# Kernel optimization log

Measured on AMD Instinct MI355X. Metric: run time of the kernel, lower is better.

The kernel has to match this reference:

```python
import jax, jax.numpy as jnp
import numpy as np

MAX_DIST = 3          # census patch radius -> 7x7 neighborhood
PATCH = 2 * MAX_DIST + 1


def _warp(img, flow):
    """Bilinear warp (Resample2d): sample img at (x + u, y + v). Coords clamped to border."""
    B, C, H, W = img.shape
    gy, gx = jnp.meshgrid(jnp.arange(H, dtype=img.dtype), jnp.arange(W, dtype=img.dtype), indexing='ij')
    x = gx[None] + flow[:, 0]           # [B,H,W]
    y = gy[None] + flow[:, 1]
    x0 = jnp.floor(x); y0 = jnp.floor(y)
    wx = x - x0; wy = y - y0            # bilinear weights
    x0i = jnp.clip(x0, 0, W - 1).astype(jnp.int32)
    x1i = jnp.clip(x0 + 1.0, 0, W - 1).astype(jnp.int32)
    y0i = jnp.clip(y0, 0, H - 1).astype(jnp.int32)
    y1i = jnp.clip(y0 + 1.0, 0, H - 1).astype(jnp.int32)

    def gather(im_b, yi, xi):           # im_b [C,H,W], yi/xi [H,W] -> [C,H,W]
        return im_b[:, yi, xi]
    g = jax.vmap(gather)
    Ia = g(img, y0i, x0i); Ib = g(img, y0i, x1i)
    Ic = g(img, y1i, x0i); Id = g(img, y1i, x1i)
    wx = wx[:, None]; wy = wy[:, None]  # [B,1,H,W]
    return Ia * (1 - wx) * (1 - wy) + Ib * wx * (1 - wy) + Ic * (1 - wx) * wy + Id * wx * wy


def _census_transform(image):
    """Ternary census transform: grayscale, extract 7x7 patches, normalized center differences."""
    gray = (0.299 * image[:, 0:1] + 0.587 * image[:, 1:2] + 0.114 * image[:, 2:3]) * 255.0
    w = jnp.eye(PATCH * PATCH, dtype=image.dtype).reshape(PATCH * PATCH, 1, PATCH, PATCH)
    patches = jax.lax.conv_general_dilated(
        gray, w, window_strides=(1, 1), padding=[(MAX_DIST, MAX_DIST)] * 2,
        dimension_numbers=('NCHW', 'OIHW', 'NCHW'))   # [B,49,H,W]
    t = patches - gray
    return t / jnp.sqrt(0.81 + t * t)


def _border_mask(B, H, W, dtype):
    m = jnp.zeros((H, W), dtype).at[MAX_DIST:H - MAX_DIST, MAX_DIST:W - MAX_DIST].set(1.0)
    return jnp.broadcast_to(m[None, None], (B, 1, H, W))


def _charbonnier(x, mask, alpha=0.45, eps=0.001):
    err = (x * x + eps * eps) ** alpha * mask
    return jnp.sum(err) / x.size


def _census_loss(im1, im2_warped, mask):
    t1 = _census_transform(im1)
    t2 = _census_transform(im2_warped)
    d = (t1 - t2) ** 2
    dist = jnp.sum(d / (0.1 + d), axis=1, keepdims=True)   # soft Hamming distance [B,1,H,W]
    B, _, H, W = dist.shape
    return _charbonnier(dist, mask * _border_mask(B, H, W, dist.dtype))


def setup_inputs() -> dict:
    key = jax.random.key(0)
    ks = jax.random.split(key, 6)
    B, H, W = 4, 320, 768
    return {
        'former': jax.random.uniform(ks[0], (B, 3, H, W), jnp.float32),
        'latter': jax.random.uniform(ks[1], (B, 3, H, W), jnp.float32),
        'disp_est_scale': jax.random.normal(ks[2], (B, 2, H, W), jnp.float32) * 3.0,
        'disp_est_scale_2': jax.random.normal(ks[3], (B, 2, H, W), jnp.float32) * 3.0,
        'fw_mask': jax.random.uniform(ks[4], (B, 1, H, W), jnp.float32),
        'bw_mask': jax.random.uniform(ks[5], (B, 1, H, W), jnp.float32),
    }


def reference(former, latter, disp_est_scale, disp_est_scale_2, fw_mask, bw_mask):
    left_est = _warp(latter, disp_est_scale)
    image_loss = _census_loss(former, left_est, fw_mask)
    right_est = _warp(former, disp_est_scale_2)
    image_loss_2 = _census_loss(latter, right_est, bw_mask)
    return (image_loss, image_loss_2)
```

## Files before the change

### kernel.cpp

```cpp
#include <hip/hip_runtime.h>

#define BB 4
#define H 320
#define W 768
#define P (H*W)
#define NPIX (BB*P)
#define P4 (P/4)
#define NP4 (NPIX/4)

#define TX 32
#define TY 8
#define TW (TX+6)
#define TH (TY+6)
#define HALO (TW*TH)
#define NBX (W/TX)
#define NBY (H/TY)
#define NBLK (NBX*NBY*BB)

typedef float f4 __attribute__((ext_vector_type(4)));

__global__ __launch_bounds__(256)
void gray_kernel(const float* __restrict__ former,
                 const float* __restrict__ latter,
                 float* __restrict__ gf, float* __restrict__ gl,
                 unsigned* __restrict__ counter) {
    int idx = blockIdx.x * blockDim.x + threadIdx.x;
    if (idx == 0) *counter = 0u;
    if (idx >= NP4) return;
    int b = idx / P4;
    int r4 = idx - b * P4;
    const float* fb = former + (size_t)b * 3 * P;
    const float* lb = latter + (size_t)b * 3 * P;
    const f4 fr = *((const f4*)fb + r4);
    const f4 fg = *((const f4*)(fb + P) + r4);
    const f4 fbl = *((const f4*)(fb + 2 * P) + r4);
    const f4 lr = *((const f4*)lb + r4);
    const f4 lg = *((const f4*)(lb + P) + r4);
    const f4 lbl = *((const f4*)(lb + 2 * P) + r4);
    f4 go, lo;
#pragma unroll
    for (int k = 0; k < 4; ++k) {
        go[k] = (0.299f * fr[k] + 0.587f * fg[k] + 0.114f * fbl[k]) * 255.f;
        lo[k] = (0.299f * lr[k] + 0.587f * lg[k] + 0.114f * lbl[k]) * 255.f;
    }
    *((f4*)gf + (size_t)b * P4 + r4) = go;
    *((f4*)gl + (size_t)b * P4 + r4) = lo;
}

__device__ __forceinline__ float bilinear(const float* __restrict__ img, float fx, float fy) {
    float x0 = floorf(fx), y0 = floorf(fy);
    float wx = fx - x0, wy = fy - y0;
    float x0c = fminf(fmaxf(x0,       0.f), (float)(W - 1));
    float x1c = fminf(fmaxf(x0 + 1.f, 0.f), (float)(W - 1));
    float y0c = fminf(fmaxf(y0,       0.f), (float)(H - 1));
    float y1c = fminf(fmaxf(y0 + 1.f, 0.f), (float)(H - 1));
    int x0i = (int)x0c, x1i = (int)x1c, y0i = (int)y0c, y1i = (int)y1c;
    float Ia = img[y0i * W + x0i], Ib = img[y0i * W + x1i];
    float Ic = img[y1i * W + x0i], Id = img[y1i * W + x1i];
    float omx = 1.f - wx, omy = 1.f - wy;
    return Ia * omx * omy + Ib * wx * omy + Ic * omx * wy + Id * wx * wy;
}

__global__ __launch_bounds__(256, 5)
void fused_kernel(const float* __restrict__ gf, const float* __restrict__ gl,
                  const float* __restrict__ flow1, const float* __restrict__ flow2,
                  const float* __restrict__ fw_mask, const float* __restrict__ bw_mask,
                  float* __restrict__ partials, unsigned* __restrict__ counter,
                  float* __restrict__ out) {
    __shared__ f4 sT[HALO];
    const int b   = blockIdx.z;
    const int tx0 = blockIdx.x * TX;
    const int ty0 = blockIdx.y * TY;
    const int tid = threadIdx.x;

    const float* pGF = gf + (size_t)b * P;
    const float* pGL = gl + (size_t)b * P;
    const float* pU1 = flow1 + (size_t)b * 2 * P;
    const float* pU2 = flow2 + (size_t)b * 2 * P;

    for (int i = tid; i < HALO; i += 256) {
        int ly = i / TW, lx = i - ly * TW;
        int gx = min(max(tx0 - 3 + lx, 0), W - 1);
        int gy = min(max(ty0 - 3 + ly, 0), H - 1);
        int o = gy * W + gx;
        float A = pGF[o];
        float C = pGL[o];
        float u1 = pU1[o], v1 = pU1[P + o];
        float u2 = pU2[o], v2 = pU2[P + o];
        float Bv = bilinear(pGL, (float)gx + u1, (float)gy + v1);
        float D  = bilinear(pGF, (float)gx + u2, (float)gy + v2);
        sT[i] = (f4){A, Bv, C, D};
    }
    __syncthreads();

    const int lx = tid & 31, ly = tid >> 5;
    const int x = tx0 + lx, y = ty0 + ly;
    float sum1 = 0.f, sum2 = 0.f;

    if (x >= 3 && x < W - 3 && y >= 3 && y < H - 3) {
        const float m1 = fw_mask[(size_t)b * P + y * W + x];
        const float m2 = bw_mask[(size_t)b * P + y * W + x];
        const int c = (ly + 3) * TW + (lx + 3);
        const f4 cv = sT[c];
        const float c1 = cv.x, c2 = cv.y, c3 = cv.z, c4 = cv.w;
        float acc1a = 0.f, acc1b = 0.f, acc2a = 0.f, acc2b = 0.f;
#pragma unroll
        for (int dy = 0; dy < 7; ++dy) {
            const int ro = (ly + dy) * TW + lx;
#pragma unroll
            for (int dx = 0; dx < 7; ++dx) {
                if (dy == 3 && dx == 3) continue;
                const f4 n = sT[ro + dx];
                const float a1 = n.x - c1, b1 = n.y - c2;
                const float qa1 = fmaf(a1, a1, 0.81f), qb1 = fmaf(b1, b1, 0.81f);
                const float pr1 = qa1 * qb1;
                const float s1 = __builtin_amdgcn_rsqf(pr1);
                const float num1 = fmaf(-0.81f, qa1 + qb1, pr1 + pr1);
                const float d1 = fmaf(num1, s1 * s1, ((a1 * b1) * s1) * -2.f);
                const float a2 = n.z - c3, b2 = n.w - c4;
                const float qa2 = fmaf(a2, a2, 0.81f), qb2 = fmaf(b2, b2, 0.81f);
                const float pr2 = qa2 * qb2;
                const float s2 = __builtin_amdgcn_rsqf(pr2);
                const float num2 = fmaf(-0.81f, qa2 + qb2, pr2 + pr2);
                const float d2 = fmaf(num2, s2 * s2, ((a2 * b2) * s2) * -2.f);
                const float e1 = d1 + 0.1f, e2 = d2 + 0.1f;
                const float ir = __builtin_amdgcn_rcpf(e1 * e2);
                const float g1 = (d1 * e2) * ir;
                const float g2 = (d2 * e1) * ir;
                if (dx & 1) { acc1a += g1; acc2a += g2; }
                else        { acc1b += g1; acc2b += g2; }
            }
        }
        const float dist1 = acc1a + acc1b;
        const float dist2 = acc2a + acc2b;
        sum1 = exp2f(0.45f * log2f(fmaf(dist1, dist1, 1e-6f))) * m1;
        sum2 = exp2f(0.45f * log2f(fmaf(dist2, dist2, 1e-6f))) * m2;
    }

#pragma unroll
    for (int off = 32; off; off >>= 1) {
        sum1 += __shfl_down(sum1, off, 64);
        sum2 += __shfl_down(sum2, off, 64);
    }
    __shared__ float red[8];
    const int wave = tid >> 6, lane = tid & 63;
    if (lane == 0) { red[wave] = sum1; red[4 + wave] = sum2; }
    __syncthreads();

    __shared__ unsigned sLast;
    if (tid == 0) {
        const int blk = (blockIdx.z * NBY + blockIdx.y) * NBX + blockIdx.x;
        __hip_atomic_store(&partials[2 * blk],     red[0] + red[1] + red[2] + red[3],
                           __ATOMIC_RELAXED, __HIP_MEMORY_SCOPE_AGENT);
        __hip_atomic_store(&partials[2 * blk + 1], red[4] + red[5] + red[6] + red[7],
                           __ATOMIC_RELAXED, __HIP_MEMORY_SCOPE_AGENT);
        asm volatile("s_waitcnt vmcnt(0)" ::: "memory");
        unsigned prev = __hip_atomic_fetch_add(counter, 1u, __ATOMIC_RELAXED,
                                               __HIP_MEMORY_SCOPE_AGENT);
        sLast = (prev == NBLK - 1) ? 1u : 0u;
    }
    __syncthreads();
    if (sLast) {
        float s1 = 0.f, s2 = 0.f;
        for (int i = tid; i < NBLK; i += 256) {
            s1 += __hip_atomic_load(&partials[2 * i],     __ATOMIC_RELAXED, __HIP_MEMORY_SCOPE_AGENT);
            s2 += __hip_atomic_load(&partials[2 * i + 1], __ATOMIC_RELAXED, __HIP_MEMORY_SCOPE_AGENT);
        }
#pragma unroll
        for (int off = 32; off; off >>= 1) {
            s1 += __shfl_down(s1, off, 64);
            s2 += __shfl_down(s2, off, 64);
        }
        __shared__ float red2[8];
        if (lane == 0) { red2[wave] = s1; red2[4 + wave] = s2; }
        __syncthreads();
        if (tid == 0) {
            out[0] = (red2[0] + red2[1] + red2[2] + red2[3]) * (1.0f / NPIX);
            out[1] = (red2[4] + red2[5] + red2[6] + red2[7]) * (1.0f / NPIX);
        }
    }
}

extern "C" void kernel_launch(void* const* d_in, const int* in_sizes, int n_in,
                              void* d_out, int out_size, void* d_ws, size_t ws_size,
                              hipStream_t stream) {
    (void)in_sizes; (void)n_in; (void)out_size; (void)ws_size;
    const float* former  = (const float*)d_in[0];
    const float* latter  = (const float*)d_in[1];
    const float* flow1   = (const float*)d_in[2];
    const float* flow2   = (const float*)d_in[3];
    const float* fw_mask = (const float*)d_in[4];
    const float* bw_mask = (const float*)d_in[5];
    float* out = (float*)d_out;
    float* ws  = (float*)d_ws;
    float* gf       = ws;
    float* gl       = ws + NPIX;
    float* partials = ws + 2 * (size_t)NPIX;
    unsigned* counter = (unsigned*)(ws + 2 * (size_t)NPIX + 2 * NBLK);

    gray_kernel<<<(NP4 + 255) / 256, 256, 0, stream>>>(former, latter, gf, gl, counter);
    fused_kernel<<<dim3(NBX, NBY, BB), 256, 0, stream>>>(gf, gl, flow1, flow2,
                                                         fw_mask, bw_mask,
                                                         partials, counter, out);
}
```

Measured before the change: 144.1 us.

## Merge gray and census kernels into persistent kernel with grid barrier

Replaces the two launches with a single persistent kernel of 1280 blocks. Each block first computes a slice of the grayscale images, then all blocks meet at a global atomic barrier, and each block then loops over several census tiles. The per-neighbor soft-Hamming maths is also simplified to compute the normalized census values directly, using one rsq per operand instead of the combined product formulation. This aims to remove a kernel launch and its gap, at the cost of a spin barrier that assumes every block is co-resident, and a memset launch to reset the counters.

Result: slower. 220.4 us (+53.0%).

```diff
diff --git a/kernel.cpp b/kernel.cpp
--- a/kernel.cpp
+++ b/kernel.cpp
@@ -17,35 +17,11 @@
 #define NBY (H/TY)
 #define NBLK (NBX*NBY*BB)
 
+#define GRID 1280
+#define TPB (NBLK/GRID)
+
 typedef float f4 __attribute__((ext_vector_type(4)));
-
-__global__ __launch_bounds__(256)
-void gray_kernel(const float* __restrict__ former,
-                 const float* __restrict__ latter,
-                 float* __restrict__ gf, float* __restrict__ gl,
-                 unsigned* __restrict__ counter) {
-    int idx = blockIdx.x * blockDim.x + threadIdx.x;
-    if (idx == 0) *counter = 0u;
-    if (idx >= NP4) return;
-    int b = idx / P4;
-    int r4 = idx - b * P4;
-    const float* fb = former + (size_t)b * 3 * P;
-    const float* lb = latter + (size_t)b * 3 * P;
-    const f4 fr = *((const f4*)fb + r4);
-    const f4 fg = *((const f4*)(fb + P) + r4);
-    const f4 fbl = *((const f4*)(fb + 2 * P) + r4);
-    const f4 lr = *((const f4*)lb + r4);
-    const f4 lg = *((const f4*)(lb + P) + r4);
-    const f4 lbl = *((const f4*)(lb + 2 * P) + r4);
-    f4 go, lo;
-#pragma unroll
-    for (int k = 0; k < 4; ++k) {
-        go[k] = (0.299f * fr[k] + 0.587f * fg[k] + 0.114f * fbl[k]) * 255.f;
-        lo[k] = (0.299f * lr[k] + 0.587f * lg[k] + 0.114f * lbl[k]) * 255.f;
-    }
-    *((f4*)gf + (size_t)b * P4 + r4) = go;
-    *((f4*)gl + (size_t)b * P4 + r4) = lo;
-}
+typedef unsigned long long u64;
 
 __device__ __forceinline__ float bilinear(const float* __restrict__ img, float fx, float fy) {
     float x0 = floorf(fx), y0 = floorf(fy);
@@ -62,102 +38,149 @@
 }
 
 __global__ __launch_bounds__(256, 5)
-void fused_kernel(const float* __restrict__ gf, const float* __restrict__ gl,
-                  const float* __restrict__ flow1, const float* __restrict__ flow2,
-                  const float* __restrict__ fw_mask, const float* __restrict__ bw_mask,
-                  float* __restrict__ partials, unsigned* __restrict__ counter,
-                  float* __restrict__ out) {
+void fused_all(const float* __restrict__ former, const float* __restrict__ latter,
+               const float* __restrict__ flow1, const float* __restrict__ flow2,
+               const float* __restrict__ fw_mask, const float* __restrict__ bw_mask,
+               float* __restrict__ gf, float* __restrict__ gl,
+               float* __restrict__ partials, unsigned* __restrict__ bar,
+               unsigned* __restrict__ done, float* __restrict__ out) {
     __shared__ f4 sT[HALO];
-    const int b   = blockIdx.z;
-    const int tx0 = blockIdx.x * TX;
-    const int ty0 = blockIdx.y * TY;
+    __shared__ float red[8];
+    __shared__ unsigned sLast;
     const int tid = threadIdx.x;
-
-    const float* pGF = gf + (size_t)b * P;
-    const float* pGL = gl + (size_t)b * P;
-    const float* pU1 = flow1 + (size_t)b * 2 * P;
-    const float* pU2 = flow2 + (size_t)b * 2 * P;
-
-    for (int i = tid; i < HALO; i += 256) {
-        int ly = i / TW, lx = i - ly * TW;
-        int gx = min(max(tx0 - 3 + lx, 0), W - 1);
-        int gy = min(max(ty0 - 3 + ly, 0), H - 1);
-        int o = gy * W + gx;
-        float A = pGF[o];
-        float C = pGL[o];
-        float u1 = pU1[o], v1 = pU1[P + o];
-        float u2 = pU2[o], v2 = pU2[P + o];
-        float Bv = bilinear(pGL, (float)gx + u1, (float)gy + v1);
-        float D  = bilinear(pGF, (float)gx + u2, (float)gy + v2);
-        sT[i] = (f4){A, Bv, C, D};
-    }
+    const int wave = tid >> 6, lane = tid & 63;
+
+    {
+        int idx = blockIdx.x * 256 + tid;
+        if (idx < NP4) {
+            int b = idx / P4;
+            int r4 = idx - b * P4;
+            const float* fb = former + (size_t)b * 3 * P;
+            const float* lb = latter + (size_t)b * 3 * P;
+            const f4 fr = *((const f4*)fb + r4);
+            const f4 fg = *((const f4*)(fb + P) + r4);
+            const f4 fbl = *((const f4*)(fb + 2 * P) + r4);
+            const f4 lr = *((const f4*)lb + r4);
+            const f4 lg = *((const f4*)(lb + P) + r4);
+            const f4 lbl = *((const f4*)(lb + 2 * P) + r4);
+            union { f4 v; u64 u[2]; } cg, cl;
+#pragma unroll
+            for (int k = 0; k < 4; ++k) {
+                cg.v[k] = (0.299f * fr[k] + 0.587f * fg[k] + 0.114f * fbl[k]) * 255.f;
+                cl.v[k] = (0.299f * lr[k] + 0.587f * lg[k] + 0.114f * lbl[k]) * 255.f;
+            }
+            u64* pg = (u64*)((f4*)gf + (size_t)b * P4 + r4);
+            u64* pl = (u64*)((f4*)gl + (size_t)b * P4 + r4);
+            __hip_atomic_store(pg,     cg.u[0], __ATOMIC_RELAXED, __HIP_MEMORY_SCOPE_AGENT);
+            __hip_atomic_store(pg + 1, cg.u[1], __ATOMIC_RELAXED, __HIP_MEMORY_SCOPE_AGENT);
+            __hip_atomic_store(pl,     cl.u[0], __ATOMIC_RELAXED, __HIP_MEMORY_SCOPE_AGENT);
+            __hip_atomic_store(pl + 1, cl.u[1], __ATOMIC_RELAXED, __HIP_MEMORY_SCOPE_AGENT);
+        }
+    }
+    asm volatile("s_waitcnt vmcnt(0)" ::: "memory");
     __syncthreads();
-
-    const int lx = tid & 31, ly = tid >> 5;
-    const int x = tx0 + lx, y = ty0 + ly;
-    float sum1 = 0.f, sum2 = 0.f;
-
-    if (x >= 3 && x < W - 3 && y >= 3 && y < H - 3) {
-        const float m1 = fw_mask[(size_t)b * P + y * W + x];
-        const float m2 = bw_mask[(size_t)b * P + y * W + x];
-        const int c = (ly + 3) * TW + (lx + 3);
-        const f4 cv = sT[c];
-        const float c1 = cv.x, c2 = cv.y, c3 = cv.z, c4 = cv.w;
-        float acc1a = 0.f, acc1b = 0.f, acc2a = 0.f, acc2b = 0.f;
-#pragma unroll
-        for (int dy = 0; dy < 7; ++dy) {
-            const int ro = (ly + dy) * TW + lx;
-#pragma unroll
-            for (int dx = 0; dx < 7; ++dx) {
-                if (dy == 3 && dx == 3) continue;
-                const f4 n = sT[ro + dx];
-                const float a1 = n.x - c1, b1 = n.y - c2;
-                const float qa1 = fmaf(a1, a1, 0.81f), qb1 = fmaf(b1, b1, 0.81f);
-                const float pr1 = qa1 * qb1;
-                const float s1 = __builtin_amdgcn_rsqf(pr1);
-                const float num1 = fmaf(-0.81f, qa1 + qb1, pr1 + pr1);
-                const float d1 = fmaf(num1, s1 * s1, ((a1 * b1) * s1) * -2.f);
-                const float a2 = n.z - c3, b2 = n.w - c4;
-                const float qa2 = fmaf(a2, a2, 0.81f), qb2 = fmaf(b2, b2, 0.81f);
-                const float pr2 = qa2 * qb2;
-                const float s2 = __builtin_amdgcn_rsqf(pr2);
-                const float num2 = fmaf(-0.81f, qa2 + qb2, pr2 + pr2);
-                const float d2 = fmaf(num2, s2 * s2, ((a2 * b2) * s2) * -2.f);
-                const float e1 = d1 + 0.1f, e2 = d2 + 0.1f;
-                const float ir = __builtin_amdgcn_rcpf(e1 * e2);
-                const float g1 = (d1 * e2) * ir;
-                const float g2 = (d2 * e1) * ir;
-                if (dx & 1) { acc1a += g1; acc2a += g2; }
-                else        { acc1b += g1; acc2b += g2; }
+    if (tid == 0) {
+        __hip_atomic_fetch_add(bar, 1u, __ATOMIC_RELAXED, __HIP_MEMORY_SCOPE_AGENT);
+        while (__hip_atomic_load(bar, __ATOMIC_RELAXED, __HIP_MEMORY_SCOPE_AGENT) < GRID)
+            __builtin_amdgcn_s_sleep(16);
+    }
+    __syncthreads();
+
+    for (int t = 0; t < TPB; ++t) {
+        const int tile = blockIdx.x * TPB + t;
+        const int bx = tile % NBX;
+        const int rem = tile / NBX;
+        const int by = rem % NBY;
+        const int b = rem / NBY;
+        const int tx0 = bx * TX, ty0 = by * TY;
+
+        const float* pGF = gf + (size_t)b * P;
+        const float* pGL = gl + (size_t)b * P;
+        const float* pU1 = flow1 + (size_t)b * 2 * P;
+        const float* pU2 = flow2 + (size_t)b * 2 * P;
+
+        for (int i = tid; i < HALO; i += 256) {
+            int ly = i / TW, lx = i - ly * TW;
+            int gx = min(max(tx0 - 3 + lx, 0), W - 1);
+            int gy = min(max(ty0 - 3 + ly, 0), H - 1);
+            int o = gy * W + gx;
+            float A = pGF[o];
+            float C = pGL[o];
+            float u1 = pU1[o], v1 = pU1[P + o];
+            float u2 = pU2[o], v2 = pU2[P + o];
+            float Bv = bilinear(pGL, (float)gx + u1, (float)gy + v1);
+            float D  = bilinear(pGF, (float)gx + u2, (float)gy + v2);
+            sT[i] = (f4){A, Bv, C, D};
+        }
+        __syncthreads();
+
+        const int lx = tid & 31, ly = tid >> 5;
+        const int x = tx0 + lx, y = ty0 + ly;
+        float sum1 = 0.f, sum2 = 0.f;
+
+        if (x >= 3 && x < W - 3 && y >= 3 && y < H - 3) {
+            const float m1 = fw_mask[(size_t)b * P + y * W + x];
+            const float m2 = bw_mask[(size_t)b * P + y * W + x];
+            const int c = (ly + 3) * TW + (lx + 3);
+            const f4 cv = sT[c];
+            const float c1 = cv.x, c2 = cv.y, c3 = cv.z, c4 = cv.w;
+            float acc1a = 0.f, acc1b = 0.f, acc2a = 0.f, acc2b = 0.f;
+#pragma unroll
+            for (int dy = 0; dy < 7; ++dy) {
+                const int ro = (ly + dy) * TW + lx;
+#pragma unroll
+                for (int dx = 0; dx < 7; ++dx) {
+                    if (dy == 3 && dx == 3) continue;
+                    const f4 n = sT[ro + dx];
+                    {
+                        const float a  = n.x - c1;
+                        const float bb = n.y - c2;
+                        const float t1 = a  * __builtin_amdgcn_rsqf(fmaf(a,  a,  0.81f));
+                        const float t2 = bb * __builtin_amdgcn_rsqf(fmaf(bb, bb, 0.81f));
+                        float d = t1 - t2; d *= d;
+                        const float r = __builtin_amdgcn_rcpf(d + 0.1f);
+                        if (dx & 1) acc1a = fmaf(d, r, acc1a);
+                        else        acc1b = fmaf(d, r, acc1b);
+                    }
+                    {
+                        const float a  = n.z - c3;
+                        const float bb = n.w - c4;
+                        const float t1 = a  * __builtin_amdgcn_rsqf(fmaf(a,  a,  0.81f));
+                        const float t2 = bb * __builtin_amdgcn_rsqf(fmaf(bb, bb, 0.81f));
+                        float d = t1 - t2; d *= d;
+                        const float r = __builtin_amdgcn_rcpf(d + 0.1f);
+                        if (dx & 1) acc2a = fmaf(d, r, acc2a);
+                        else        acc2b = fmaf(d, r, acc2b);
+                    }
+                }
             }
-        }
-        const float dist1 = acc1a + acc1b;
-        const float dist2 = acc2a + acc2b;
-        sum1 = exp2f(0.45f * log2f(fmaf(dist1, dist1, 1e-6f))) * m1;
-        sum2 = exp2f(0.45f * log2f(fmaf(dist2, dist2, 1e-6f))) * m2;
-    }
-
-#pragma unroll
-    for (int off = 32; off; off >>= 1) {
-        sum1 += __shfl_down(sum1, off, 64);
-        sum2 += __shfl_down(sum2, off, 64);
-    }
-    __shared__ float red[8];
-    const int wave = tid >> 6, lane = tid & 63;
-    if (lane == 0) { red[wave] = sum1; red[4 + wave] = sum2; }
-    __syncthreads();
-
-    __shared__ unsigned sLast;
+            const float dist1 = acc1a + acc1b;
+            const float dist2 = acc2a + acc2b;
+            sum1 = exp2f(0.45f * log2f(fmaf(dist1, dist1, 1e-6f))) * m1;
+            sum2 = exp2f(0.45f * log2f(fmaf(dist2, dist2, 1e-6f))) * m2;
+        }
+
+#pragma unroll
+        for (int off = 32; off; off >>= 1) {
+            sum1 += __shfl_down(sum1, off, 64);
+            sum2 += __shfl_down(sum2, off, 64);
+        }
+        if (lane == 0) { red[wave] = sum1; red[4 + wave] = sum2; }
+        __syncthreads();
+        if (tid == 0) {
+            __hip_atomic_store(&partials[2 * tile],     red[0] + red[1] + red[2] + red[3],
+                               __ATOMIC_RELAXED, __HIP_MEMORY_SCOPE_AGENT);
+            __hip_atomic_store(&partials[2 * tile + 1], red[4] + red[5] + red[6] + red[7],
+                               __ATOMIC_RELAXED, __HIP_MEMORY_SCOPE_AGENT);
+        }
+        __syncthreads();
+    }
+
     if (tid == 0) {
-        const int blk = (blockIdx.z * NBY + blockIdx.y) * NBX + blockIdx.x;
-        __hip_atomic_store(&partials[2 * blk],     red[0] + red[1] + red[2] + red[3],
-                           __ATOMIC_RELAXED, __HIP_MEMORY_SCOPE_AGENT);
-        __hip_atomic_store(&partials[2 * blk + 1], red[4] + red[5] + red[6] + red[7],
-                           __ATOMIC_RELAXED, __HIP_MEMORY_SCOPE_AGENT);
         asm volatile("s_waitcnt vmcnt(0)" ::: "memory");
-        unsigned prev = __hip_atomic_fetch_add(counter, 1u, __ATOMIC_RELAXED,
+        unsigned prev = __hip_atomic_fetch_add(done, 1u, __ATOMIC_RELAXED,
                                                __HIP_MEMORY_SCOPE_AGENT);
-        sLast = (prev == NBLK - 1) ? 1u : 0u;
+        sLast = (prev == GRID - 1) ? 1u : 0u;
     }
     __syncthreads();
     if (sLast) {
@@ -193,13 +216,15 @@
     const float* bw_mask = (const float*)d_in[5];
     float* out = (float*)d_out;
     float* ws  = (float*)d_ws;
-    float* gf       = ws;
-    float* gl       = ws + NPIX;
-    float* partials = ws + 2 * (size_t)NPIX;
-    unsigned* counter = (unsigned*)(ws + 2 * (size_t)NPIX + 2 * NBLK);
-
-    gray_kernel<<<(NP4 + 255) / 256, 256, 0, stream>>>(former, latter, gf, gl, counter);
-    fused_kernel<<<dim3(NBX, NBY, BB), 256, 0, stream>>>(gf, gl, flow1, flow2,
-                                                         fw_mask, bw_mask,
-                                                         partials, counter, out);
+    float* partials   = ws;
+    unsigned* bar     = (unsigned*)(ws + 2 * NBLK);
+    unsigned* done    = bar + 1;
+    float* gf         = ws + 2 * NBLK + 4;
+    float* gl         = gf + NPIX;
+
+    hipMemsetAsync(bar, 0, 2 * sizeof(unsigned), stream);
+    void* args_unused = nullptr; (void)args_unused;
+    fused_all<<<GRID, 256, 0, stream>>>(former, latter, flow1, flow2,
+                                        fw_mask, bw_mask, gf, gl,
+                                        partials, bar, done, out);
 }
```
